# Kernel optimization log

Hardware: AMD Instinct MI355X
Metric: run time of the kernel (lower is better)

## Reference

```python
import jax, jax.numpy as jnp
import numpy as np

C, H, W = 512, 64, 64
N_PROP = 2000
ROI = 7          # roi_size
FEAT_STRIDE = 16
IMG = 1024.0
NEG = jnp.finfo(jnp.float32).min


def setup_inputs() -> dict:
    key = jax.random.key(0)
    k1, k2, k3, k4, k5 = jax.random.split(key, 5)
    features = jax.random.normal(k1, (1, C, H, W), dtype=jnp.float32)
    # proposals (x1, y1, x2, y2) in image pixel coords; width/height >= 32 px
    # so that after /feat_stride flooring each ROI spans >= 2 feature cells.
    x1 = jax.random.uniform(k2, (N_PROP,)) * (IMG - 64.0)
    y1 = jax.random.uniform(k3, (N_PROP,)) * (IMG - 64.0)
    bw = 32.0 + jax.random.uniform(k4, (N_PROP,)) * (IMG / 3.0)
    bh = 32.0 + jax.random.uniform(k5, (N_PROP,)) * (IMG / 3.0)
    x2 = jnp.minimum(x1 + bw, IMG - 1.0)
    y2 = jnp.minimum(y1 + bh, IMG - 1.0)
    proposals = jnp.stack([x1, y1, x2, y2], axis=1).astype(jnp.float32)
    return {"features": features, "proposals": proposals}


def _adaptive_bins(lo, length):
    # PyTorch AdaptiveMaxPool bin edges: start=floor(i*L/R), end=ceil((i+1)*L/R)
    i = jnp.arange(ROI)
    starts = lo + (i * length) // ROI
    ends = lo + ((i + 1) * length + ROI - 1) // ROI
    return starts, ends


def _pool_one(feats, prop):
    # prop: int32 [4] = (x1, y1, x2, y2) in feature-map coords
    x1, y1, x2, y2 = prop[0], prop[1], prop[2], prop[3]
    hs, he = _adaptive_bins(y1, y2 - y1)    # [ROI]
    ws, we = _adaptive_bins(x1, x2 - x1)    # [ROI]
    h_idx = jnp.arange(H)
    w_idx = jnp.arange(W)
    mask_h = (h_idx[None, :] >= hs[:, None]) & (h_idx[None, :] < he[:, None])  # [ROI,H]
    mask_w = (w_idx[None, :] >= ws[:, None]) & (w_idx[None, :] < we[:, None])  # [ROI,W]
    # stage 1: max over w per output column -> [C, H, ROI]
    t1 = jnp.max(jnp.where(mask_w[None, None, :, :], feats[:, :, None, :], NEG), axis=-1)
    # stage 2: max over h per output row -> [C, ROI, ROI]
    out = jnp.max(jnp.where(mask_h[None, :, :, None], t1[:, None, :, :], NEG), axis=2)
    return out


def reference(features, proposals):
    feats = jnp.squeeze(features, axis=0)                              # [C,H,W]
    props = jnp.floor(proposals / FEAT_STRIDE).astype(jnp.int32)       # [N,4]
    roi = jax.lax.map(lambda p: _pool_one(feats, p), props)            # [N,C,ROI,ROI]
    return roi.astype(jnp.float32)
```

## Files before the change

### kernel.cpp

```cpp
#include <hip/hip_runtime.h>


#define NCH   512
#define FH    64
#define FW    64
#define NPROP 2000
#define ROI   7
#define OUT_PER_PROP (NCH * ROI * ROI)
#define NCHUNK 8
#define CCH    64
#define TABF   (FH * FW * CCH)
#define CHUNK_F (4 * TABF)
#define TAB_BYTES ((size_t)NCHUNK * CHUNK_F * 4)
#define ROWF2  (FW * CCH / 2)

typedef float floatx4 __attribute__((ext_vector_type(4)));

__global__ __launch_bounds__(256) void prep2d_kernel(
    const float* __restrict__ f,
    float* __restrict__ ws)
{
    __shared__ float tA[64][65];
    __shared__ float tB[64][65];
    const int b  = blockIdx.x;
    const int q  = b & 7;
    const int h  = b >> 3;
    const int h2 = min(h + 1, FH - 1);
    const int c0 = q * CCH;
    const int tw = threadIdx.x & 63;
    const int tg = threadIdx.x >> 6;
#pragma unroll
    for (int r = 0; r < 16; ++r) {
        const int cl = r * 4 + tg;
        tA[cl][tw] = f[(size_t)(c0 + cl) * (FH * FW) + h  * FW + tw];
        tB[cl][tw] = f[(size_t)(c0 + cl) * (FH * FW) + h2 * FW + tw];
    }
    __syncthreads();
    float* __restrict__ T = ws + (size_t)q * CHUNK_F + h * (FW * CCH);
#pragma unroll
    for (int r = 0; r < 16; ++r) {
        const int wl = r * 4 + tg;
        const int w1 = min(wl + 1, FW - 1);
        const float a0 = tA[tw][wl], a1 = tA[tw][w1];
        const float b0 = tB[tw][wl], b1 = tB[tw][w1];
        const float m01 = fmaxf(a0, a1);
        const float m10 = fmaxf(a0, b0);
        const float m11 = fmaxf(m01, fmaxf(b0, b1));
        const int o = wl * CCH + tw;
        T[o]            = a0;
        T[TABF + o]     = m01;
        T[2 * TABF + o] = m10;
        T[3 * TABF + o] = m11;
    }
}

__device__ __forceinline__ void compute_bins(
    const float* __restrict__ props, int n,
    int* s_hs, int* s_he, int* s_ws, int* s_we)
{
    if (threadIdx.x < ROI) {
        const int i = threadIdx.x;
        const int x1 = (int)floorf(props[n * 4 + 0] * 0.0625f);
        const int y1 = (int)floorf(props[n * 4 + 1] * 0.0625f);
        const int x2 = (int)floorf(props[n * 4 + 2] * 0.0625f);
        const int y2 = (int)floorf(props[n * 4 + 3] * 0.0625f);
        const int Lh = y2 - y1;
        const int Lw = x2 - x1;
        s_hs[i] = max(y1 + (i * Lh) / ROI, 0);
        s_he[i] = min(y1 + ((i + 1) * Lh + (ROI - 1)) / ROI, FH);
        s_ws[i] = max(x1 + (i * Lw) / ROI, 0);
        s_we[i] = min(x1 + ((i + 1) * Lw + (ROI - 1)) / ROI, FW);
    }
}

template<bool H3, bool W3>
__device__ __forceinline__ void accum2d(
    const float2* __restrict__ t2,
    int baseA, int baseB, int baseC,
    const int sA[ROI], const int sB[ROI], const int sC[ROI],
    float m0[ROI], float m1[ROI])
{
    float2 rAA[ROI], rAB[ROI], rBA[ROI], rBB[ROI];
#pragma unroll
    for (int j = 0; j < ROI; ++j) {
        rAA[j] = t2[(size_t)(baseA + sA[j])];
        rAB[j] = t2[(size_t)(baseA + sB[j])];
        rBA[j] = t2[(size_t)(baseB + sA[j])];
        rBB[j] = t2[(size_t)(baseB + sB[j])];
    }
#pragma unroll
    for (int j = 0; j < ROI; ++j) {
        float x0 = fmaxf(fmaxf(rAA[j].x, rAB[j].x), fmaxf(rBA[j].x, rBB[j].x));
        float x1 = fmaxf(fmaxf(rAA[j].y, rAB[j].y), fmaxf(rBA[j].y, rBB[j].y));
        if (W3) {
            const float2 uAC = t2[(size_t)(baseA + sC[j])];
            const float2 uBC = t2[(size_t)(baseB + sC[j])];
            x0 = fmaxf(x0, fmaxf(uAC.x, uBC.x));
            x1 = fmaxf(x1, fmaxf(uAC.y, uBC.y));
        }
        if (H3) {
            const float2 uCA = t2[(size_t)(baseC + sA[j])];
            const float2 uCB = t2[(size_t)(baseC + sB[j])];
            x0 = fmaxf(x0, fmaxf(uCA.x, uCB.x));
            x1 = fmaxf(x1, fmaxf(uCA.y, uCB.y));
            if (W3) {
                const float2 uCC = t2[(size_t)(baseC + sC[j])];
                x0 = fmaxf(x0, uCC.x);
                x1 = fmaxf(x1, uCC.y);
            }
        }
        m0[j] = x0;
        m1[j] = x1;
    }
}

__global__ __launch_bounds__(256, 4) void roipool_2d_kernel(
    const float* __restrict__ tabs,
    const float* __restrict__ props,
    float* __restrict__ out)
{
    const int b = blockIdx.x;
    const int q = b & 7;
    const int n = b >> 3;

    __shared__ int s_hs[ROI], s_he[ROI], s_ws[ROI], s_we[ROI];
    __shared__ __align__(16) float s_stage[CCH * 49];
    compute_bins(props, n, s_hs, s_he, s_ws, s_we);
    __syncthreads();

    int sA[ROI], sB[ROI], sC[ROI];
    bool w5 = false, h5 = false;
#pragma unroll
    for (int j = 0; j < ROI; ++j) {
        const int wsj = __builtin_amdgcn_readfirstlane(s_ws[j]);
        const int wej = __builtin_amdgcn_readfirstlane(s_we[j]);
        const int len = wej - wsj;
        const int kwo = (len >= 2) ? (TABF / 2) : 0;
        const int wB  = (len >= 3) ? (wej - 2) : wsj;
        const int wC  = (len == 5) ? (wsj + 2) : wsj;
        sA[j] = kwo + wsj * (CCH / 2);
        sB[j] = kwo + wB  * (CCH / 2);
        sC[j] = kwo + wC  * (CCH / 2);
        w5 = w5 || (len == 5);
        const int hl = __builtin_amdgcn_readfirstlane(s_he[j]) -
                       __builtin_amdgcn_readfirstlane(s_hs[j]);
        h5 = h5 || (hl == 5);
    }

    const int slot = threadIdx.x >> 5;
    const int bi   = min(slot, 6);
    const int c2   = threadIdx.x & 31;

    if (slot < 7) {
        const int hsb  = s_hs[bi];
        const int heb  = s_he[bi];
        const int hlen = heb - hsb;
        const int khoff = (hlen >= 2) ? TABF : 0;
        const int hB   = (hlen >= 3) ? (heb - 2) : hsb;
        const int hC   = (hlen == 5) ? (hsb + 2) : hsb;

        const float2* __restrict__ t2 = (const float2*)tabs + (size_t)q * (CHUNK_F / 2);
        const int baseA = khoff + hsb * ROWF2 + c2;
        const int baseB = khoff + hB  * ROWF2 + c2;
        const int baseC = khoff + hC  * ROWF2 + c2;

        float m0[ROI], m1[ROI];
        if (h5) {
            if (w5) accum2d<true,  true >(t2, baseA, baseB, baseC, sA, sB, sC, m0, m1);
            else    accum2d<true,  false>(t2, baseA, baseB, baseC, sA, sB, sC, m0, m1);
        } else {
            if (w5) accum2d<false, true >(t2, baseA, baseB, baseC, sA, sB, sC, m0, m1);
            else    accum2d<false, false>(t2, baseA, baseB, baseC, sA, sB, sC, m0, m1);
        }

#pragma unroll
        for (int j = 0; j < ROI; ++j) {
            s_stage[(2 * c2)     * 49 + bi * 7 + j] = m0[j];
            s_stage[(2 * c2 + 1) * 49 + bi * 7 + j] = m1[j];
        }
    }
    __syncthreads();

    floatx4* __restrict__ dsto = (floatx4*)(out + (size_t)n * OUT_PER_PROP + q * (CCH * 49));
    const floatx4* __restrict__ srco = (const floatx4*)s_stage;
    for (int i = threadIdx.x; i < (CCH * 49 / 4); i += 256)
        __builtin_nontemporal_store(srco[i], dsto + i);
}

__global__ __launch_bounds__(256) void roipool_direct_kernel(
    const float* __restrict__ feats,
    const float* __restrict__ props,
    float* __restrict__ out)
{
    const int n = blockIdx.x;
    __shared__ int s_hs[ROI], s_he[ROI], s_ws[ROI], s_we[ROI];
    compute_bins(props, n, s_hs, s_he, s_ws, s_we);
    __syncthreads();
    const float NEG = -3.402823466e+38f;
    const int base = blockIdx.y * (256 * ROI);
    float* outn = out + (size_t)n * OUT_PER_PROP;
#pragma unroll
    for (int k = 0; k < ROI; ++k) {
        const int idx = base + k * 256 + threadIdx.x;
        const int c   = idx / (ROI * ROI);
        const int bin = idx - c * (ROI * ROI);
        const int bi  = bin / ROI;
        const int bj  = bin - bi * ROI;
        float acc = NEG;
        for (int h = s_hs[bi]; h < s_he[bi]; ++h)
            for (int w = s_ws[bj]; w < s_we[bj]; ++w)
                acc = fmaxf(acc, feats[(size_t)c * (FH * FW) + h * FW + w]);
        outn[idx] = acc;
    }
}

extern "C" void kernel_launch(void* const* d_in, const int* in_sizes, int n_in,
                              void* d_out, int out_size, void* d_ws, size_t ws_size,
                              hipStream_t stream) {
    const float* feats = (const float*)d_in[0];
    const float* props = (const float*)d_in[1];
    float* out = (float*)d_out;
    float* ws  = (float*)d_ws;

    if (ws_size >= TAB_BYTES) {
        prep2d_kernel<<<dim3(FH * NCHUNK), 256, 0, stream>>>(feats, ws);
        roipool_2d_kernel<<<dim3(NPROP * NCHUNK), 256, 0, stream>>>(ws, props, out);
    } else {
        roipool_direct_kernel<<<dim3(NPROP, ROI * 2), 256, 0, stream>>>(feats, props, out);
    }
}
```

Before: 72.40 us.

## Assign channel chunks to XCDs via atomic work-claiming for L2 locality

Instead of a fixed blockIdx-to-(chunk, proposal) mapping, each block reads its XCC id and atomically claims the next proposal from a per-chunk counter, preferring the chunk matching its XCD. This aims to keep each 4 MB channel-chunk table resident in one XCD's L2 rather than spreading all chunks across every XCD's cache. It adds a global atomic per block and a barrier, plus a counter reset in the prep kernel, and relies on the workspace being large enough to hold the counters.

After: 200.6 us. 2.77x slower.

```diff
diff --git a/kernel.cpp b/kernel.cpp
--- a/kernel.cpp
+++ b/kernel.cpp
@@ -16,10 +16,19 @@
 
 typedef float floatx4 __attribute__((ext_vector_type(4)));
 
+__device__ __forceinline__ int get_xcc() {
+    int x;
+    asm("s_getreg_b32 %0, hwreg(HW_REG_XCC_ID)" : "=s"(x));
+    return x & 7;
+}
+
 __global__ __launch_bounds__(256) void prep2d_kernel(
     const float* __restrict__ f,
-    float* __restrict__ ws)
-{
+    float* __restrict__ ws,
+    int* __restrict__ cnt)
+{
+    if (blockIdx.x == 0 && threadIdx.x < NCHUNK) cnt[threadIdx.x] = 0;
+
     __shared__ float tA[64][65];
     __shared__ float tB[64][65];
     const int b  = blockIdx.x;
@@ -117,11 +126,24 @@
 __global__ __launch_bounds__(256, 4) void roipool_2d_kernel(
     const float* __restrict__ tabs,
     const float* __restrict__ props,
-    float* __restrict__ out)
-{
-    const int b = blockIdx.x;
-    const int q = b & 7;
-    const int n = b >> 3;
+    float* __restrict__ out,
+    int* __restrict__ cnt)
+{
+    __shared__ int s_claim;
+    if (threadIdx.x == 0) {
+        const int q0 = get_xcc();
+        int claim = -1;
+        for (int t = 0; t < NCHUNK; ++t) {
+            const int qq = (q0 + t) & 7;
+            const int nn = atomicAdd(&cnt[qq], 1);
+            if (nn < NPROP) { claim = (qq << 16) | nn; break; }
+        }
+        s_claim = claim;
+    }
+    __syncthreads();
+    if (s_claim < 0) return;
+    const int q = s_claim >> 16;
+    const int n = s_claim & 0xffff;
 
     __shared__ int s_hs[ROI], s_he[ROI], s_ws[ROI], s_we[ROI];
     __shared__ __align__(16) float s_stage[CCH * 49];
@@ -222,9 +244,10 @@
     float* out = (float*)d_out;
     float* ws  = (float*)d_ws;
 
-    if (ws_size >= TAB_BYTES) {
-        prep2d_kernel<<<dim3(FH * NCHUNK), 256, 0, stream>>>(feats, ws);
-        roipool_2d_kernel<<<dim3(NPROP * NCHUNK), 256, 0, stream>>>(ws, props, out);
+    if (ws_size >= TAB_BYTES + NCHUNK * sizeof(int)) {
+        int* cnt = (int*)((char*)d_ws + TAB_BYTES);
+        prep2d_kernel<<<dim3(FH * NCHUNK), 256, 0, stream>>>(feats, ws, cnt);
+        roipool_2d_kernel<<<dim3(NPROP * NCHUNK), 256, 0, stream>>>(ws, props, out, cnt);
     } else {
         roipool_direct_kernel<<<dim3(NPROP, ROI * 2), 256, 0, stream>>>(feats, props, out);
     }
```
